# Kernel optimization log

Hardware: AMD Instinct MI355X
Metric: run time of the kernel (lower is better)

Reference implementation:

```python
import jax, jax.numpy as jnp
import numpy as np

T, B, H, E, V = 128, 64, 512, 256, 32000
UNK = 2
EPS = 1e-10


def setup_inputs() -> dict:
    key = jax.random.key(0)
    ks = jax.random.split(key, 16)
    s = 0.02
    return {
        "u_enc_out": jax.random.normal(ks[0], (T, B, H), jnp.float32),
        "z_tm1": jax.random.randint(ks[1], (1, B), 0, V),
        "last_hidden": jax.random.normal(ks[2], (1, B, H), jnp.float32),
        "u_input": jax.random.randint(ks[3], (T, B), 0, V),
        "emb": jax.random.normal(ks[4], (V, E), jnp.float32) * s,
        "attn_W": jax.random.normal(ks[5], (H, 2 * H), jnp.float32) * s,
        "attn_b": jnp.zeros((H,), jnp.float32),
        "attn_v": jax.random.normal(ks[6], (H,), jnp.float32) * (1.0 / np.sqrt(H)),
        "gru_Wih": jax.random.normal(ks[7], (3 * H, H + E), jnp.float32) * s,
        "gru_Whh": jax.random.normal(ks[8], (3 * H, H), jnp.float32) * s,
        "gru_bih": jnp.zeros((3 * H,), jnp.float32),
        "gru_bhh": jnp.zeros((3 * H,), jnp.float32),
        "proj_W": jax.random.normal(ks[9], (V, 2 * H), jnp.float32) * s,
        "proj_b": jnp.zeros((V,), jnp.float32),
        "copy1_W": jax.random.normal(ks[10], (H, H), jnp.float32) * s,
        "copy1_b": jnp.zeros((H,), jnp.float32),
    }


def _copy_logscore(raw, u_input):
    # raw: [B,T] copy scores; u_input: [T,B] int ids
    # Faithful to: log(bmm(exp(raw - max), sparse_one_hot_with_1e-10_floor)) + max
    cmax = jnp.max(raw, axis=1, keepdims=True)            # [B,1]
    ex = jnp.exp(raw - cmax)                              # [B,T]
    idx = u_input.T                                       # [B,T]
    idx = jnp.where(idx == UNK, V + jnp.arange(T)[None, :], idx)
    mask = (u_input.T != 0).astype(ex.dtype)
    total = jnp.sum(ex, axis=1)                           # [B] (all t, incl. ignored)
    scat = jax.vmap(lambda e, i: jnp.zeros((V + T,), ex.dtype).at[i].add(e))(ex * mask, idx)
    return jnp.log(EPS * total[:, None] + (1.0 - EPS) * scat) + cmax  # [B,V+T]


def reference(u_enc_out, z_tm1, last_hidden, u_input, emb, attn_W, attn_b, attn_v,
              gru_Wih, gru_Whh, gru_bih, gru_bhh, proj_W, proj_b, copy1_W, copy1_b):
    enc = jnp.transpose(u_enc_out, (1, 0, 2))             # [B,T,H]
    h = last_hidden[0]                                    # [B,H]
    # Attn: energy = tanh(Linear([h;enc])), score = v . energy, softmax over T
    Hrep = jnp.broadcast_to(h[:, None, :], enc.shape)
    energy = jnp.tanh(jnp.einsum('bti,hi->bth', jnp.concatenate([Hrep, enc], -1), attn_W) + attn_b)
    alpha = jax.nn.softmax(jnp.einsum('h,bth->bt', attn_v, energy), axis=1)
    ctx = jnp.einsum('bt,bth->bh', alpha, enc)            # [B,H]
    # GRU step (pytorch gate order r,z,n)
    x = jnp.concatenate([emb[z_tm1[0]], ctx], axis=-1)    # [B,E+H]
    gi = x @ gru_Wih.T + gru_bih
    gh = h @ gru_Whh.T + gru_bhh
    i_r, i_z, i_n = jnp.split(gi, 3, axis=-1)
    h_r, h_z, h_n = jnp.split(gh, 3, axis=-1)
    r = jax.nn.sigmoid(i_r + h_r)
    z = jax.nn.sigmoid(i_z + h_z)
    n = jnp.tanh(i_n + r * h_n)
    h_new = (1.0 - z) * n + z * h                         # [B,H]
    gru_out = h_new[None]                                 # [1,B,H]
    new_hidden = h_new[None]
    # generation score
    gen_score = jnp.concatenate([h_new, ctx], -1) @ proj_W.T + proj_b  # [B,V]
    # copy score
    cs = jnp.tanh(jnp.einsum('bth,ih->bti', enc, copy1_W) + copy1_b)   # [B,T,H]
    raw = jnp.einsum('bth,bh->bt', cs, h_new)             # [B,T]
    u_copy = _copy_logscore(raw, u_input)                 # [B,V+T]
    scores = jax.nn.softmax(jnp.concatenate([gen_score, u_copy], axis=1), axis=1)
    g, c = scores[:, :V], scores[:, V:]                   # [B,V], [B,V+T]
    proba = jnp.concatenate([g + c[:, :V], c[:, V:]], axis=1)  # [B,V+T]
    return gru_out, new_hidden, proba
```

## Files before the change

kernel.cpp:

```cpp
#include <hip/hip_runtime.h>
#include <math.h>

#define T_ 128
#define B_ 64
#define H_ 512
#define E_ 256
#define V_ 32000
#define VT_ (V_ + T_)
#define UNK_ 2
#define EPS_ 1e-10f
#define NP_ (V_ / 64)

typedef __attribute__((ext_vector_type(8))) _Float16 half8;
typedef __attribute__((ext_vector_type(2))) _Float16 half2v;
typedef __attribute__((ext_vector_type(4))) float floatx4;

#define NB_ZERO 32
#define NB_CVTE 2048
#define NB_CVTA 512
#define NB_CVTC 512
#define NB_WHM  8
#define NB_CVTW 2048
#define NB_XE   64
#define NB_XH   128
#define NB_BC   8
#define NB_PRO (NB_ZERO + NB_CVTE + NB_CVTA + NB_CVTC + NB_WHM + NB_CVTW + NB_XE + NB_XH + NB_BC)

__global__ __launch_bounds__(256) void prologue_k(
        const float* __restrict__ u_enc, const float* __restrict__ attn_W,
        const float* __restrict__ copy1_W, const float* __restrict__ last_h,
        const float* __restrict__ attn_b, const float* __restrict__ emb,
        const int* __restrict__ z, const float* __restrict__ Wih,
        const float* __restrict__ Whh, const float* __restrict__ bih,
        const float* __restrict__ bhh,
        float* __restrict__ zbase, _Float16* __restrict__ enc_bh,
        _Float16* __restrict__ Wb_attn, _Float16* __restrict__ Wb_copy,
        float* __restrict__ Wh, _Float16* __restrict__ Wcat,
        _Float16* __restrict__ xg, float* __restrict__ bcat) {
    int bid = blockIdx.x, tid = threadIdx.x;
    if (bid < NB_ZERO) { zbase[bid * 256 + tid] = 0.f; return; }
    bid -= NB_ZERO;
    if (bid < NB_CVTE) {
        int idx8 = bid * 256 + tid;
        int i = idx8 * 8;
        float4 a = *(const float4*)(u_enc + i);
        float4 b4 = *(const float4*)(u_enc + i + 4);
        half8 o;
        o[0] = (_Float16)a.x; o[1] = (_Float16)a.y; o[2] = (_Float16)a.z; o[3] = (_Float16)a.w;
        o[4] = (_Float16)b4.x; o[5] = (_Float16)b4.y; o[6] = (_Float16)b4.z; o[7] = (_Float16)b4.w;
        int h8 = idx8 & 63;
        int tb = idx8 >> 6;
        int b = tb & 63, t = tb >> 6;
        *(half8*)(enc_bh + ((size_t)(b * T_ + t) * H_) + h8 * 8) = o;
        return;
    }
    bid -= NB_CVTE;
    if (bid < NB_CVTA) {
        int c = tid * 2;
        float2 v = *(const float2*)(attn_W + (size_t)bid * 1024 + 512 + c);
        Wb_attn[bid * 512 + c]     = (_Float16)v.x;
        Wb_attn[bid * 512 + c + 1] = (_Float16)v.y;
        return;
    }
    bid -= NB_CVTA;
    if (bid < NB_CVTC) {
        int c = tid * 2;
        float2 v = *(const float2*)(copy1_W + (size_t)bid * 512 + c);
        Wb_copy[bid * 512 + c]     = (_Float16)v.x;
        Wb_copy[bid * 512 + c + 1] = (_Float16)v.y;
        return;
    }
    bid -= NB_CVTC;
    if (bid < NB_WHM) {
        int lane = tid & 63, wave = tid >> 6;
        int n0 = bid * 64 + wave * 16;
        int coln = lane & 15;
        int kq = (lane >> 4) * 8;
        const float* wrow = attn_W + (size_t)(n0 + coln) * 1024 + kq;
        const float* arow0 = last_h + kq;
        floatx4 acc[4] = {};
        #pragma unroll 4
        for (int k0 = 0; k0 < 512; k0 += 32) {
            const float4* wb = (const float4*)(wrow + k0);
            float4 w0 = wb[0], w1 = wb[1];
            half8 fb;
            fb[0] = (_Float16)w0.x; fb[1] = (_Float16)w0.y; fb[2] = (_Float16)w0.z; fb[3] = (_Float16)w0.w;
            fb[4] = (_Float16)w1.x; fb[5] = (_Float16)w1.y; fb[6] = (_Float16)w1.z; fb[7] = (_Float16)w1.w;
            #pragma unroll
            for (int mi = 0; mi < 4; ++mi) {
                const float4* ab = (const float4*)(arow0 + (size_t)(mi * 16 + coln) * 512 + k0);
                float4 a0 = ab[0], a1 = ab[1];
                half8 fa;
                fa[0] = (_Float16)a0.x; fa[1] = (_Float16)a0.y; fa[2] = (_Float16)a0.z; fa[3] = (_Float16)a0.w;
                fa[4] = (_Float16)a1.x; fa[5] = (_Float16)a1.y; fa[6] = (_Float16)a1.z; fa[7] = (_Float16)a1.w;
                acc[mi] = __builtin_amdgcn_mfma_f32_16x16x32_f16(fa, fb, acc[mi], 0, 0, 0);
            }
        }
        int rbase = (lane >> 4) * 4;
        float bias = attn_b[n0 + coln];
        #pragma unroll
        for (int mi = 0; mi < 4; ++mi)
            #pragma unroll
            for (int r = 0; r < 4; ++r)
                Wh[(size_t)(mi * 16 + rbase + r) * 512 + n0 + coln] = acc[mi][r] + bias;
        return;
    }
    bid -= NB_WHM;
    if (bid < NB_CVTW) {
        int mp = bid;
        int q  = (mp >> 4) & 3;
        int hh = (mp >> 6) * 16 + (mp & 15);
        #pragma unroll
        for (int j = 0; j < 5; ++j) {
            int c = j * 256 + tid;
            float w;
            if (q == 0)      w = (c < 768) ? Wih[(size_t)hh * 768 + c]
                                           : Whh[(size_t)hh * 512 + (c - 768)];
            else if (q == 1) w = (c < 768) ? Wih[(size_t)(512 + hh) * 768 + c]
                                           : Whh[(size_t)(512 + hh) * 512 + (c - 768)];
            else if (q == 2) w = (c < 768) ? Wih[(size_t)(1024 + hh) * 768 + c] : 0.f;
            else             w = (c >= 768) ? Whh[(size_t)(1024 + hh) * 512 + (c - 768)] : 0.f;
            Wcat[(size_t)mp * 1280 + c] = (_Float16)w;
        }
        return;
    }
    bid -= NB_CVTW;
    if (bid < NB_XE) {
        int idx = bid * 256 + tid;
        int bb = idx >> 8, c = idx & 255;
        xg[bb * 1280 + c] = (_Float16)emb[(size_t)z[bb] * E_ + c];
        return;
    }
    bid -= NB_XE;
    if (bid < NB_XH) {
        int idx = bid * 256 + tid;
        int bb = idx >> 9, c = idx & 511;
        xg[bb * 1280 + 768 + c] = (_Float16)last_h[bb * H_ + c];
        return;
    }
    bid -= NB_XH;
    {
        int mp = bid * 256 + tid;
        int q  = (mp >> 4) & 3;
        int hh = (mp >> 6) * 16 + (mp & 15);
        float v2;
        if (q == 0)      v2 = bih[hh] + bhh[hh];
        else if (q == 1) v2 = bih[512 + hh] + bhh[512 + hh];
        else if (q == 2) v2 = bih[1024 + hh];
        else             v2 = bhh[1024 + hh];
        bcat[mp] = v2;
    }
}

__global__ __launch_bounds__(256) void enc_dual_k(
        const _Float16* __restrict__ enc_bh,
        const _Float16* __restrict__ Wa,
        const _Float16* __restrict__ Wc,
        const float* __restrict__ Wh,
        const float* __restrict__ attn_v,
        const float* __restrict__ copy1_b,
        float* __restrict__ score,
        _Float16* __restrict__ cs) {
    __shared__ _Float16 As[64 * 512];
    int bid = blockIdx.x;
    int xcd = bid & 7, loc = bid >> 3;
    int xt = xcd * 16 + (loc & 15);
    int yt = loc >> 4;
    int r0 = xt * 64;
    int b  = r0 >> 7;
    int tid = threadIdx.x;
    int lane = tid & 63, wave = tid >> 6;
    const half8* src = (const half8*)(enc_bh + (size_t)r0 * H_);
    #pragma unroll
    for (int i = 0; i < 16; ++i) {
        int G = i * 256 + tid;
        half8 v = src[G];
        int r = G >> 6, s = G & 63;
        *(half8*)&As[(size_t)(((r << 6) | (s ^ (r & 7))) << 3)] = v;
    }
    __syncthreads();
    int n0 = yt * 64 + wave * 16;
    int coln = lane & 15;
    int g = lane >> 4;
    const _Float16* wra = Wa + (size_t)(n0 + coln) * H_ + g * 8;
    const _Float16* wrc = Wc + (size_t)(n0 + coln) * H_ + g * 8;
    floatx4 acca[4] = {}, accc[4] = {};
    #pragma unroll 4
    for (int k0 = 0; k0 < H_; k0 += 32) {
        half8 fba = *(const half8*)(wra + k0);
        half8 fbc = *(const half8*)(wrc + k0);
        #pragma unroll
        for (int mi = 0; mi < 4; ++mi) {
            int r = mi * 16 + coln;
            half8 fa = *(const half8*)&As[((size_t)r << 9) +
                          ((((k0 >> 3) + g) ^ (coln & 7)) << 3)];
            acca[mi] = __builtin_amdgcn_mfma_f32_16x16x32_f16(fa, fba, acca[mi], 0, 0, 0);
            accc[mi] = __builtin_amdgcn_mfma_f32_16x16x32_f16(fa, fbc, accc[mi], 0, 0, 0);
        }
    }
    int col = n0 + coln;
    float addt = Wh[b * H_ + col];
    float av   = attn_v[col];
    float cb   = copy1_b[col];
    int rbase = g * 4;
    #pragma unroll
    for (int mi = 0; mi < 4; ++mi)
        #pragma unroll
        for (int r = 0; r < 4; ++r) {
            int row = r0 + mi * 16 + rbase + r;
            float x = acca[mi][r] + addt;
            float t2 = __expf(2.f * x);
            float v = av * ((t2 - 1.f) / (t2 + 1.f));
            v += __shfl_xor(v, 1);
            v += __shfl_xor(v, 2);
            v += __shfl_xor(v, 4);
            v += __shfl_xor(v, 8);
            if (coln == 0) atomicAdd(&score[row], v);
            float y = accc[mi][r] + cb;
            float t3 = __expf(2.f * y);
            cs[(size_t)row * H_ + col] = (_Float16)((t3 - 1.f) / (t3 + 1.f));
        }
}

__global__ __launch_bounds__(256) void softctx_k(
        const float* __restrict__ score, const _Float16* __restrict__ enc_bh,
        _Float16* __restrict__ xcat, _Float16* __restrict__ xg) {
    __shared__ float al[T_];
    __shared__ float red[T_];
    int b = blockIdx.x, tid = threadIdx.x;
    float v = (tid < T_) ? score[b * T_ + tid] : -1e30f;
    if (tid < T_) red[tid] = v;
    __syncthreads();
    for (int s = 64; s > 0; s >>= 1) { if (tid < s) red[tid] = fmaxf(red[tid], red[tid + s]); __syncthreads(); }
    float m = red[0]; __syncthreads();
    float e = (tid < T_) ? __expf(v - m) : 0.f;
    if (tid < T_) red[tid] = e;
    __syncthreads();
    for (int s = 64; s > 0; s >>= 1) { if (tid < s) red[tid] += red[tid + s]; __syncthreads(); }
    if (tid < T_) al[tid] = e / red[0];
    __syncthreads();
    const half2v* ebase = (const half2v*)(enc_bh + (size_t)b * T_ * H_) + tid;
    float s0 = 0.f, s1 = 0.f;
    #pragma unroll 8
    for (int t = 0; t < T_; ++t) {
        half2v u = ebase[(size_t)t * 256];
        float a = al[t];
        s0 += a * (float)u[0];
        s1 += a * (float)u[1];
    }
    int h0 = tid * 2;
    half2v o; o[0] = (_Float16)s0; o[1] = (_Float16)s1;
    *(half2v*)(xcat + b * 1024 + 512 + h0) = o;
    *(half2v*)(xg + b * 1280 + 256 + h0)   = o;
}

__global__ __launch_bounds__(512) void grucat_k(
        const _Float16* __restrict__ xg,
        const _Float16* __restrict__ Wcat,
        const float* __restrict__ bcat,
        const float* __restrict__ hprev,
        float* __restrict__ out,
        _Float16* __restrict__ xcat) {
    __shared__ float Lt[8][64][17];
    int tid = threadIdx.x;
    int lane = tid & 63, wave = tid >> 6;
    int q = wave & 3, khalf = wave >> 2;
    int n0 = blockIdx.x * 64 + q * 16;
    int coln = lane & 15;
    int kq  = (lane >> 4) * 8;
    int kbase = khalf * 640;
    const _Float16* wrow  = Wcat + (size_t)(n0 + coln) * 1280 + kbase + kq;
    const _Float16* abase = xg + kbase + kq;
    floatx4 acc[4] = {};
    #pragma unroll 5
    for (int k0 = 0; k0 < 640; k0 += 32) {
        half8 fb = *(const half8*)(wrow + k0);
        #pragma unroll
        for (int mi = 0; mi < 4; ++mi) {
            half8 fa = *(const half8*)(abase + (size_t)(mi * 16 + coln) * 1280 + k0);
            acc[mi] = __builtin_amdgcn_mfma_f32_16x16x32_f16(fa, fb, acc[mi], 0, 0, 0);
        }
    }
    int rbase = (lane >> 4) * 4;
    #pragma unroll
    for (int mi = 0; mi < 4; ++mi)
        #pragma unroll
        for (int r = 0; r < 4; ++r)
            Lt[wave][mi * 16 + rbase + r][coln] = acc[mi][r];
    __syncthreads();
    int HB = blockIdx.x * 16;
    #pragma unroll
    for (int p = tid; p < 1024; p += 512) {
        int b = p >> 4, i = p & 15;
        float G0 = Lt[0][b][i] + Lt[4][b][i] + bcat[blockIdx.x * 64 + i];
        float G1 = Lt[1][b][i] + Lt[5][b][i] + bcat[blockIdx.x * 64 + 16 + i];
        float G2 = Lt[2][b][i] + Lt[6][b][i] + bcat[blockIdx.x * 64 + 32 + i];
        float G3 = Lt[3][b][i] + Lt[7][b][i] + bcat[blockIdx.x * 64 + 48 + i];
        float rr = 1.f / (1.f + __expf(-G0));
        float zz = 1.f / (1.f + __expf(-G1));
        float nn = tanhf(G2 + rr * G3);
        float h  = hprev[b * H_ + HB + i];
        float hv = (1.f - zz) * nn + zz * h;
        out[b * H_ + HB + i] = hv;
        out[B_ * H_ + b * H_ + HB + i] = hv;
        xcat[b * 1024 + HB + i] = (_Float16)hv;
    }
}

__global__ __launch_bounds__(256) void proj_stats_k(
        const _Float16* __restrict__ xcat,
        const float* __restrict__ Wp,
        const float* __restrict__ bp,
        float* __restrict__ gen,
        float* __restrict__ mpart, float* __restrict__ lpart) {
    __shared__ float m_lds[4][64];
    __shared__ float l_lds[4][64];
    int lane = threadIdx.x & 63;
    int wave = threadIdx.x >> 6;
    int n0 = (blockIdx.x * 4 + wave) * 16;
    int coln = lane & 15;
    int kq  = (lane >> 4) * 8;
    const float* wrow = Wp + (size_t)(n0 + coln) * 1024 + kq;
    const _Float16* abase = xcat + kq;
    floatx4 acc[4] = {};
    #pragma unroll 8
    for (int k0 = 0; k0 < 1024; k0 += 32) {
        const float4* wb = (const float4*)(wrow + k0);
        float4 w0 = wb[0], w1 = wb[1];
        half8 fb;
        fb[0] = (_Float16)w0.x; fb[1] = (_Float16)w0.y; fb[2] = (_Float16)w0.z; fb[3] = (_Float16)w0.w;
        fb[4] = (_Float16)w1.x; fb[5] = (_Float16)w1.y; fb[6] = (_Float16)w1.z; fb[7] = (_Float16)w1.w;
        #pragma unroll
        for (int mi = 0; mi < 4; ++mi) {
            half8 fa = *(const half8*)(abase + (size_t)(mi * 16 + coln) * 1024 + k0);
            acc[mi] = __builtin_amdgcn_mfma_f32_16x16x32_f16(fa, fb, acc[mi], 0, 0, 0);
        }
    }
    int rbase = (lane >> 4) * 4;
    float bias = bp[n0 + coln];
    #pragma unroll
    for (int mi = 0; mi < 4; ++mi)
        #pragma unroll
        for (int r = 0; r < 4; ++r) {
            int brow = mi * 16 + rbase + r;
            float x = acc[mi][r] + bias;
            gen[(size_t)brow * V_ + n0 + coln] = x;
            float mm = x;
            mm = fmaxf(mm, __shfl_xor(mm, 1));
            mm = fmaxf(mm, __shfl_xor(mm, 2));
            mm = fmaxf(mm, __shfl_xor(mm, 4));
            mm = fmaxf(mm, __shfl_xor(mm, 8));
            float e = __expf(x - mm);
            e += __shfl_xor(e, 1);
            e += __shfl_xor(e, 2);
            e += __shfl_xor(e, 4);
            e += __shfl_xor(e, 8);
            if (coln == 0) { m_lds[wave][brow] = mm; l_lds[wave][brow] = e; }
        }
    __syncthreads();
    if (threadIdx.x < 64) {
        int bb = threadIdx.x;
        float M = m_lds[0][bb], L = l_lds[0][bb];
        #pragma unroll
        for (int w = 1; w < 4; ++w) {
            float m2 = m_lds[w][bb], l2 = l_lds[w][bb];
            float nm = fmaxf(M, m2);
            L = L * __expf(M - nm) + l2 * __expf(m2 - nm);
            M = nm;
        }
        mpart[bb * NP_ + blockIdx.x] = M;
        lpart[bb * NP_ + blockIdx.x] = L;
    }
}

__global__ __launch_bounds__(256) void raw_epi_k(
        const _Float16* __restrict__ cs, const float* __restrict__ hnew,
        const int* __restrict__ u_input,
        const float* __restrict__ mpart, const float* __restrict__ lpart,
        float* __restrict__ scat, float* __restrict__ params) {
    __shared__ float rawS[T_];
    __shared__ float red[T_];
    __shared__ float ms[256], ls[256];
    int b = blockIdx.x, tid = threadIdx.x;
    int lane = tid & 63, wave = tid >> 6;
    const float4* hp = (const float4*)(hnew + b * H_ + lane * 8);
    float4 ha = hp[0], hb = hp[1];
    #pragma unroll 4
    for (int i = 0; i < 32; ++i) {
        int t = wave * 32 + i;
        half8 c8 = *(const half8*)(cs + (size_t)(b * T_ + t) * H_ + lane * 8);
        float s = (float)c8[0] * ha.x + (float)c8[1] * ha.y + (float)c8[2] * ha.z + (float)c8[3] * ha.w
                + (float)c8[4] * hb.x + (float)c8[5] * hb.y + (float)c8[6] * hb.z + (float)c8[7] * hb.w;
        #pragma unroll
        for (int off = 32; off > 0; off >>= 1) s += __shfl_down(s, off);
        if (lane == 0) rawS[t] = s;
    }
    __syncthreads();
    int t = tid;
    float v = (t < T_) ? rawS[t] : -1e30f;
    if (t < T_) red[t] = v;
    __syncthreads();
    for (int s = 64; s > 0; s >>= 1) { if (t < s) red[t] = fmaxf(red[t], red[t + s]); __syncthreads(); }
    float cm = red[0]; __syncthreads();
    float e = (t < T_) ? __expf(v - cm) : 0.f;
    if (t < T_) red[t] = e;
    __syncthreads();
    for (int s = 64; s > 0; s >>= 1) { if (t < s) red[t] += red[t + s]; __syncthreads(); }
    float tot = red[0]; __syncthreads();
    int id = (t < T_) ? u_input[t * B_ + b] : 0;
    size_t j = (size_t)b * VT_ + ((id == UNK_) ? (V_ + t) : id);
    if (id != 0) scat[j] = 0.f;
    __syncthreads();
    if (id != 0) atomicAdd(&scat[j], e);
    if (t < T_) red[t] = (id != 0) ? e : 0.f;
    __syncthreads();
    for (int s = 64; s > 0; s >>= 1) { if (t < s) red[t] += red[t + s]; __syncthreads(); }
    float ssum = red[0]; __syncthreads();
    float sv = (id != 0) ? scat[j] : 0.f;
    if (t < T_) red[t] = sv;
    __syncthreads();
    for (int s = 64; s > 0; s >>= 1) { if (t < s) red[t] = fmaxf(red[t], red[t + s]); __syncthreads(); }
    float smax = red[0]; __syncthreads();
    float M = -1e30f, L = 0.f;
    for (int s = t; s < NP_; s += 256) {
        float m2 = mpart[b * NP_ + s], l2 = lpart[b * NP_ + s];
        float nm = fmaxf(M, m2);
        L = L * __expf(M - nm) + l2 * __expf(m2 - nm);
        M = nm;
    }
    ms[t] = M; ls[t] = L;
    __syncthreads();
    for (int s = 128; s > 0; s >>= 1) {
        if (t < s) {
            float m2 = ms[t + s], l2 = ls[t + s];
            float nm = fmaxf(ms[t], m2);
            ls[t] = ls[t] * __expf(ms[t] - nm) + l2 * __expf(m2 - nm);
            ms[t] = nm;
        }
        __syncthreads();
    }
    if (t == 0) {
        float Mg = ms[0], Zg = ls[0];
        float umax = cm + logf(EPS_ * tot + (1.f - EPS_) * smax);
        float M2 = fmaxf(Mg, umax);
        float coef = __expf(cm - M2);
        float Z = Zg * __expf(Mg - M2) + coef * (EPS_ * tot * (float)VT_ + (1.f - EPS_) * ssum);
        float invZ = 1.f / Z;
        params[b * 4 + 0] = M2;
        params[b * 4 + 1] = invZ;
        params[b * 4 + 2] = coef * EPS_ * tot * invZ;
        params[b * 4 + 3] = coef * (1.f - EPS_) * invZ;
    }
}

__global__ __launch_bounds__(256) void write_k(const float* __restrict__ gen,
                                               const float* __restrict__ params,
                                               float* __restrict__ proba) {
    int b = blockIdx.y;
    int i4 = blockIdx.x * 256 + threadIdx.x;
    if (i4 >= VT_ / 4) return;
    float M = params[b * 4], invZ = params[b * 4 + 1], addc = params[b * 4 + 2];
    int j = i4 * 4;
    float4 p;
    if (j < V_) {
        float4 g = *(const float4*)(gen + (size_t)b * V_ + j);
        p.x = addc + __expf(g.x - M) * invZ;
        p.y = addc + __expf(g.y - M) * invZ;
        p.z = addc + __expf(g.z - M) * invZ;
        p.w = addc + __expf(g.w - M) * invZ;
    } else {
        p.x = p.y = p.z = p.w = addc;
    }
    *(float4*)(proba + (size_t)b * VT_ + j) = p;
}

__global__ void fix_k(const float* __restrict__ gen, const float* __restrict__ scat,
                      const int* __restrict__ u_input, const float* __restrict__ params,
                      float* __restrict__ proba) {
    int b = blockIdx.x, t = threadIdx.x;
    int id = u_input[t * B_ + b];
    if (id == 0) return;
    int j = (id == UNK_) ? (V_ + t) : id;
    float M = params[b * 4], invZ = params[b * 4 + 1];
    float addc = params[b * 4 + 2], scoef = params[b * 4 + 3];
    float p = addc + scoef * scat[(size_t)b * VT_ + j];
    if (j < V_) p += __expf(gen[(size_t)b * V_ + j] - M) * invZ;
    proba[(size_t)b * VT_ + j] = p;
}

extern "C" void kernel_launch(void* const* d_in, const int* in_sizes, int n_in,
                              void* d_out, int out_size, void* d_ws, size_t ws_size,
                              hipStream_t stream) {
    const float* u_enc   = (const float*)d_in[0];
    const int*   z_tm1   = (const int*)d_in[1];
    const float* last_h  = (const float*)d_in[2];
    const int*   u_input = (const int*)d_in[3];
    const float* emb     = (const float*)d_in[4];
    const float* attn_W  = (const float*)d_in[5];
    const float* attn_b  = (const float*)d_in[6];
    const float* attn_v  = (const float*)d_in[7];
    const float* gru_Wih = (const float*)d_in[8];
    const float* gru_Whh = (const float*)d_in[9];
    const float* gru_bih = (const float*)d_in[10];
    const float* gru_bhh = (const float*)d_in[11];
    const float* proj_W  = (const float*)d_in[12];
    const float* proj_b  = (const float*)d_in[13];
    const float* copy1_W = (const float*)d_in[14];
    const float* copy1_b = (const float*)d_in[15];
    float* out = (float*)d_out;

    float* ws    = (float*)d_ws;
    float* score = ws;
    float* gen   = score + B_ * T_;
    float* scat  = gen + (size_t)B_ * V_;
    float* Wh    = scat + (size_t)B_ * VT_;
    float* mpart = Wh + B_ * H_;
    float* lpart = mpart + B_ * NP_;
    float* params= lpart + B_ * NP_;
    float* bcat  = params + B_ * 4;
    _Float16* xcat  = (_Float16*)(bcat + 2048);
    _Float16* xg    = xcat + B_ * 1024;
    _Float16* enc_bh = xg + B_ * 1280;
    _Float16* Wb_attn = enc_bh + (size_t)T_ * B_ * H_;
    _Float16* Wb_copy = Wb_attn + H_ * H_;
    _Float16* Wcat  = Wb_copy + H_ * H_;
    _Float16* cs    = Wcat + 2048 * 1280;

    prologue_k<<<NB_PRO, 256, 0, stream>>>(u_enc, attn_W, copy1_W, last_h, attn_b,
                                           emb, z_tm1, gru_Wih, gru_Whh, gru_bih, gru_bhh,
                                           score, enc_bh, Wb_attn, Wb_copy, Wh, Wcat, xg, bcat);

    enc_dual_k<<<1024, 256, 0, stream>>>(enc_bh, Wb_attn, Wb_copy, Wh, attn_v, copy1_b,
                                         score, cs);

    softctx_k<<<B_, 256, 0, stream>>>(score, enc_bh, xcat, xg);

    grucat_k<<<32, 512, 0, stream>>>(xg, Wcat, bcat, last_h, out, xcat);

    proj_stats_k<<<NP_, 256, 0, stream>>>(xcat, proj_W, proj_b, gen, mpart, lpart);

    raw_epi_k<<<B_, 256, 0, stream>>>(cs, out, u_input, mpart, lpart, scat, params);

    float* proba = out + 2 * B_ * H_;
    write_k<<<dim3((VT_ / 4 + 255) / 256, B_), 256, 0, stream>>>(gen, params, proba);
    fix_k<<<B_, T_, 0, stream>>>(gen, scat, u_input, params, proba);
}
```

Baseline: 381.6 us.

## Read fp32 encoder outputs directly, drop fp16 transposed staging copy

Removes the prologue pass that converted u_enc_out into a transposed fp16 [B,T,H] buffer. enc_dual_k now loads fp32 rows straight from the [T,B,H] input, converting to fp16 while filling shared memory, and softctx_k reads fp32 with a strided layout. The Wh = last_hidden·attn_W matmul is also switched from an MFMA tile to a simple per-wave dot-product reduction across 8192 blocks. This avoids a 16 MB read plus 8 MB write round trip, in exchange for strided, wider fp32 reads in the consumer kernels.

```diff
diff --git a/kernel.cpp b/kernel.cpp
--- a/kernel.cpp
+++ b/kernel.cpp
@@ -16,45 +16,29 @@
 typedef __attribute__((ext_vector_type(4))) float floatx4;
 
 #define NB_ZERO 32
-#define NB_CVTE 2048
 #define NB_CVTA 512
 #define NB_CVTC 512
-#define NB_WHM  8
+#define NB_WH   8192
 #define NB_CVTW 2048
 #define NB_XE   64
 #define NB_XH   128
 #define NB_BC   8
-#define NB_PRO (NB_ZERO + NB_CVTE + NB_CVTA + NB_CVTC + NB_WHM + NB_CVTW + NB_XE + NB_XH + NB_BC)
+#define NB_PRO (NB_ZERO + NB_CVTA + NB_CVTC + NB_WH + NB_CVTW + NB_XE + NB_XH + NB_BC)
 
 __global__ __launch_bounds__(256) void prologue_k(
-        const float* __restrict__ u_enc, const float* __restrict__ attn_W,
+        const float* __restrict__ attn_W,
         const float* __restrict__ copy1_W, const float* __restrict__ last_h,
         const float* __restrict__ attn_b, const float* __restrict__ emb,
         const int* __restrict__ z, const float* __restrict__ Wih,
         const float* __restrict__ Whh, const float* __restrict__ bih,
         const float* __restrict__ bhh,
-        float* __restrict__ zbase, _Float16* __restrict__ enc_bh,
+        float* __restrict__ zbase,
         _Float16* __restrict__ Wb_attn, _Float16* __restrict__ Wb_copy,
         float* __restrict__ Wh, _Float16* __restrict__ Wcat,
         _Float16* __restrict__ xg, float* __restrict__ bcat) {
     int bid = blockIdx.x, tid = threadIdx.x;
     if (bid < NB_ZERO) { zbase[bid * 256 + tid] = 0.f; return; }
     bid -= NB_ZERO;
-    if (bid < NB_CVTE) {
-        int idx8 = bid * 256 + tid;
-        int i = idx8 * 8;
-        float4 a = *(const float4*)(u_enc + i);
-        float4 b4 = *(const float4*)(u_enc + i + 4);
-        half8 o;
-        o[0] = (_Float16)a.x; o[1] = (_Float16)a.y; o[2] = (_Float16)a.z; o[3] = (_Float16)a.w;
-        o[4] = (_Float16)b4.x; o[5] = (_Float16)b4.y; o[6] = (_Float16)b4.z; o[7] = (_Float16)b4.w;
-        int h8 = idx8 & 63;
-        int tb = idx8 >> 6;
-        int b = tb & 63, t = tb >> 6;
-        *(half8*)(enc_bh + ((size_t)(b * T_ + t) * H_) + h8 * 8) = o;
-        return;
-    }
-    bid -= NB_CVTE;
     if (bid < NB_CVTA) {
         int c = tid * 2;
         float2 v = *(const float2*)(attn_W + (size_t)bid * 1024 + 512 + c);
@@ -71,41 +55,24 @@
         return;
     }
     bid -= NB_CVTC;
-    if (bid < NB_WHM) {
-        int lane = tid & 63, wave = tid >> 6;
-        int n0 = bid * 64 + wave * 16;
-        int coln = lane & 15;
-        int kq = (lane >> 4) * 8;
-        const float* wrow = attn_W + (size_t)(n0 + coln) * 1024 + kq;
-        const float* arow0 = last_h + kq;
-        floatx4 acc[4] = {};
-        #pragma unroll 4
-        for (int k0 = 0; k0 < 512; k0 += 32) {
-            const float4* wb = (const float4*)(wrow + k0);
-            float4 w0 = wb[0], w1 = wb[1];
-            half8 fb;
-            fb[0] = (_Float16)w0.x; fb[1] = (_Float16)w0.y; fb[2] = (_Float16)w0.z; fb[3] = (_Float16)w0.w;
-            fb[4] = (_Float16)w1.x; fb[5] = (_Float16)w1.y; fb[6] = (_Float16)w1.z; fb[7] = (_Float16)w1.w;
-            #pragma unroll
-            for (int mi = 0; mi < 4; ++mi) {
-                const float4* ab = (const float4*)(arow0 + (size_t)(mi * 16 + coln) * 512 + k0);
-                float4 a0 = ab[0], a1 = ab[1];
-                half8 fa;
-                fa[0] = (_Float16)a0.x; fa[1] = (_Float16)a0.y; fa[2] = (_Float16)a0.z; fa[3] = (_Float16)a0.w;
-                fa[4] = (_Float16)a1.x; fa[5] = (_Float16)a1.y; fa[6] = (_Float16)a1.z; fa[7] = (_Float16)a1.w;
-                acc[mi] = __builtin_amdgcn_mfma_f32_16x16x32_f16(fa, fb, acc[mi], 0, 0, 0);
-            }
-        }
-        int rbase = (lane >> 4) * 4;
-        float bias = attn_b[n0 + coln];
-        #pragma unroll
-        for (int mi = 0; mi < 4; ++mi)
-            #pragma unroll
-            for (int r = 0; r < 4; ++r)
-                Wh[(size_t)(mi * 16 + rbase + r) * 512 + n0 + coln] = acc[mi][r] + bias;
+    if (bid < NB_WH) {
+        int wid = bid * 4 + (tid >> 6), lane = tid & 63;
+        int b = wid >> 9, m = wid & 511;
+        const float4* wr = (const float4*)(attn_W + (size_t)m * 1024);
+        const float4* xr = (const float4*)(last_h + b * 512);
+        float s = 0.f;
+        #pragma unroll
+        for (int i = 0; i < 2; ++i) {
+            int k = lane + i * 64;
+            float4 w = wr[k], x = xr[k];
+            s += w.x * x.x + w.y * x.y + w.z * x.z + w.w * x.w;
+        }
+        #pragma unroll
+        for (int off = 32; off > 0; off >>= 1) s += __shfl_down(s, off);
+        if (lane == 0) Wh[b * 512 + m] = s + attn_b[m];
         return;
     }
-    bid -= NB_WHM;
+    bid -= NB_WH;
     if (bid < NB_CVTW) {
         int mp = bid;
         int q  = (mp >> 4) & 3;
@@ -153,7 +120,7 @@
 }
 
 __global__ __launch_bounds__(256) void enc_dual_k(
-        const _Float16* __restrict__ enc_bh,
+        const float* __restrict__ u_enc,
         const _Float16* __restrict__ Wa,
         const _Float16* __restrict__ Wc,
         const float* __restrict__ Wh,
@@ -166,16 +133,21 @@
     int xcd = bid & 7, loc = bid >> 3;
     int xt = xcd * 16 + (loc & 15);
     int yt = loc >> 4;
-    int r0 = xt * 64;
-    int b  = r0 >> 7;
+    int b  = xt >> 1;
+    int t0 = (xt & 1) * 64;
+    int r0 = b * T_ + t0;
     int tid = threadIdx.x;
     int lane = tid & 63, wave = tid >> 6;
-    const half8* src = (const half8*)(enc_bh + (size_t)r0 * H_);
+    const float* srcb = u_enc + (size_t)t0 * B_ * H_ + (size_t)b * H_;
     #pragma unroll
     for (int i = 0; i < 16; ++i) {
         int G = i * 256 + tid;
-        half8 v = src[G];
         int r = G >> 6, s = G & 63;
+        const float4* p = (const float4*)(srcb + (size_t)r * B_ * H_ + s * 8);
+        float4 a0 = p[0], a1 = p[1];
+        half8 v;
+        v[0] = (_Float16)a0.x; v[1] = (_Float16)a0.y; v[2] = (_Float16)a0.z; v[3] = (_Float16)a0.w;
+        v[4] = (_Float16)a1.x; v[5] = (_Float16)a1.y; v[6] = (_Float16)a1.z; v[7] = (_Float16)a1.w;
         *(half8*)&As[(size_t)(((r << 6) | (s ^ (r & 7))) << 3)] = v;
     }
     __syncthreads();
@@ -223,7 +195,7 @@
 }
 
 __global__ __launch_bounds__(256) void softctx_k(
-        const float* __restrict__ score, const _Float16* __restrict__ enc_bh,
+        const float* __restrict__ score, const float* __restrict__ u_enc,
         _Float16* __restrict__ xcat, _Float16* __restrict__ xg) {
     __shared__ float al[T_];
     __shared__ float red[T_];
@@ -239,14 +211,14 @@
     for (int s = 64; s > 0; s >>= 1) { if (tid < s) red[tid] += red[tid + s]; __syncthreads(); }
     if (tid < T_) al[tid] = e / red[0];
     __syncthreads();
-    const half2v* ebase = (const half2v*)(enc_bh + (size_t)b * T_ * H_) + tid;
+    const float2* ebase = (const float2*)(u_enc + (size_t)b * H_) + tid;
     float s0 = 0.f, s1 = 0.f;
     #pragma unroll 8
     for (int t = 0; t < T_; ++t) {
-        half2v u = ebase[(size_t)t * 256];
+        float2 u = ebase[(size_t)t * (B_ * H_ / 2)];
         float a = al[t];
-        s0 += a * (float)u[0];
-        s1 += a * (float)u[1];
+        s0 += a * u.x;
+        s1 += a * u.y;
     }
     int h0 = tid * 2;
     half2v o; o[0] = (_Float16)s0; o[1] = (_Float16)s1;
@@ -520,20 +492,19 @@
     float* bcat  = params + B_ * 4;
     _Float16* xcat  = (_Float16*)(bcat + 2048);
     _Float16* xg    = xcat + B_ * 1024;
-    _Float16* enc_bh = xg + B_ * 1280;
-    _Float16* Wb_attn = enc_bh + (size_t)T_ * B_ * H_;
+    _Float16* Wb_attn = xg + B_ * 1280;
     _Float16* Wb_copy = Wb_attn + H_ * H_;
     _Float16* Wcat  = Wb_copy + H_ * H_;
     _Float16* cs    = Wcat + 2048 * 1280;
 
-    prologue_k<<<NB_PRO, 256, 0, stream>>>(u_enc, attn_W, copy1_W, last_h, attn_b,
+    prologue_k<<<NB_PRO, 256, 0, stream>>>(attn_W, copy1_W, last_h, attn_b,
                                            emb, z_tm1, gru_Wih, gru_Whh, gru_bih, gru_bhh,
-                                           score, enc_bh, Wb_attn, Wb_copy, Wh, Wcat, xg, bcat);
-
-    enc_dual_k<<<1024, 256, 0, stream>>>(enc_bh, Wb_attn, Wb_copy, Wh, attn_v, copy1_b,
+                                           score, Wb_attn, Wb_copy, Wh, Wcat, xg, bcat);
+
+    enc_dual_k<<<1024, 256, 0, stream>>>(u_enc, Wb_attn, Wb_copy, Wh, attn_v, copy1_b,
                                          score, cs);
 
-    softctx_k<<<B_, 256, 0, stream>>>(score, enc_bh, xcat, xg);
+    softctx_k<<<B_, 256, 0, stream>>>(score, u_enc, xcat, xg);
 
     grucat_k<<<32, 512, 0, stream>>>(xg, Wcat, bcat, last_h, out, xcat);
 
```

New measurement: 372.8 us. 1.02x faster.
